# Performance work log

Measured on AMD Instinct MI355X. Metric: run time of the kernel, lower is better.

The kernel has to match this reference:

```python
import jax, jax.numpy as jnp
import numpy as np

N_NODES = 50000
N_FEAT = 256
N_HID = 256
N_CLASS = 40
N_EDGES = 800000


def setup_inputs() -> dict:
    key = jax.random.key(0)
    ks = jax.random.split(key, 12)
    x = jax.random.normal(ks[0], (N_NODES, N_FEAT), dtype=jnp.float32)
    edge_index = jax.random.randint(ks[1], (2, N_EDGES), 0, N_NODES, dtype=jnp.int64)
    def glorot(k, fan_in, fan_out):
        s = jnp.sqrt(6.0 / (fan_in + fan_out)).astype(jnp.float32)
        return jax.random.uniform(k, (fan_in, fan_out), jnp.float32, -s, s)
    return {
        "x": x,
        "edge_index": edge_index,
        "W1": glorot(ks[2], N_FEAT, N_HID), "b1": jnp.zeros((N_HID,), jnp.float32),
        "W2": glorot(ks[3], N_HID, N_HID), "b2": jnp.zeros((N_HID,), jnp.float32),
        "W3": glorot(ks[4], N_HID, N_HID), "b3": jnp.zeros((N_HID,), jnp.float32),
        "W4": glorot(ks[5], N_HID, N_CLASS), "b4": jnp.zeros((N_CLASS,), jnp.float32),
    }


def _gcn_norm(edge_index, num_nodes):
    # add self-loops, compute symmetric normalization (PyG gcn_norm)
    loop = jnp.arange(num_nodes, dtype=edge_index.dtype)
    src = jnp.concatenate([edge_index[0], loop])
    dst = jnp.concatenate([edge_index[1], loop])
    deg = jax.ops.segment_sum(jnp.ones_like(dst, dtype=jnp.float32), dst,
                              num_segments=num_nodes)
    dis = jnp.where(deg > 0, jax.lax.rsqrt(deg), 0.0)
    norm = dis[src] * dis[dst]  # [E + N]
    return src, dst, norm


def _gcn_conv(x, W, b, src, dst, norm, num_nodes):
    h = x @ W  # dense transform first (out_channels <= in_channels)
    msg = norm[:, None] * h[src]  # gather + scale
    out = jax.ops.segment_sum(msg, dst, num_segments=num_nodes)  # scatter-add
    return out + b


def reference(x, edge_index, W1, b1, W2, b2, W3, b3, W4, b4):
    n = x.shape[0]
    src, dst, norm = _gcn_norm(edge_index, n)
    h = jax.nn.relu(_gcn_conv(x, W1, b1, src, dst, norm, n))
    # dropout is identity in eval mode
    h = jax.nn.relu(_gcn_conv(h, W2, b2, src, dst, norm, n))
    h = jax.nn.relu(_gcn_conv(h, W3, b3, src, dst, norm, n))
    out = _gcn_conv(h, W4, b4, src, dst, norm, n)
    return out
```

## Files before the change

### kernel.cpp

```cpp
#include <hip/hip_runtime.h>

#define NN 50000
#define NF 256
#define NH 256
#define NC 40
#define NE 800000
#define CAP 64

typedef _Float16 f16x8 __attribute__((ext_vector_type(8)));
typedef float f32x4 __attribute__((ext_vector_type(4)));

__device__ __forceinline__ float f16f(unsigned short u) {
  union { unsigned short u; _Float16 h; } a; a.u = u;
  return (float)a.h;
}
__device__ __forceinline__ unsigned short f16u(float f) {
  union { unsigned short u; _Float16 h; } a; a.h = (_Float16)f;
  return a.u;
}

__device__ __forceinline__ void gl16(const void* g, void* l) {
  __builtin_amdgcn_global_load_lds(
      (const __attribute__((address_space(1))) unsigned int*)g,
      (__attribute__((address_space(3))) unsigned int*)l, 16, 0, 0);
}


__global__ void bucket_kernel(const int* __restrict__ src, const int* __restrict__ dst,
                              int* __restrict__ cnt, int* __restrict__ bucket) {
  int e = blockIdx.x * blockDim.x + threadIdx.x;
  if (e < NE) {
    int d = dst[e], s = src[e];
    int c = atomicAdd(&cnt[d], 1);
    if (c < CAP) bucket[(size_t)d * CAP + c] = s;
  }
}

__global__ void prep_kernel(const int* __restrict__ cnt, float* __restrict__ dis,
                            const float* __restrict__ W1, const float* __restrict__ W2,
                            const float* __restrict__ W3, const float* __restrict__ W4,
                            unsigned short* __restrict__ Wt1, unsigned short* __restrict__ Wt2,
                            unsigned short* __restrict__ Wt3, unsigned short* __restrict__ Wt4) {
  int idx = blockIdx.x * blockDim.x + threadIdx.x;
  if (idx < 262144) {
    const float* W; unsigned short* Wt; int N;
    if (idx < 65536)       { W = W1; Wt = Wt1; N = 256; }
    else if (idx < 131072) { W = W2; Wt = Wt2; N = 256; idx -= 65536; }
    else if (idx < 196608) { W = W3; Wt = Wt3; N = 256; idx -= 131072; }
    else                   { W = W4; Wt = Wt4; N = 40;  idx -= 196608; }
    int n = idx >> 8, k = idx & 255;
    float v = (n < N) ? W[k * N + n] : 0.0f;
    Wt[idx] = f16u(v);
  } else {
    int i = idx - 262144;
    if (i < NN) dis[i] = rsqrtf((float)(cnt[i] + 1));
  }
}


template <int NSTORE, bool AF32>
__global__ __launch_bounds__(256, 4) void gemm_f16(
    const void* __restrict__ Ain, const unsigned short* __restrict__ Bt,
    unsigned short* __restrict__ Cout, int M) {
  __shared__ unsigned short ldsA[64 * 64];
  __shared__ unsigned short ldsB[256 * 64];

  int tid = threadIdx.x;
  int rowBase = blockIdx.x * 64;
  int w = tid >> 6, lane = tid & 63;
  int l15 = lane & 15, l4 = lane >> 4;

  f32x4 acc[4][4] = {};

  for (int kt = 0; kt < 4; ++kt) {
#pragma unroll
    for (int c = 0; c < 2; ++c) {
      int gi = c * 256 + tid;
      int row = gi >> 3, gp = gi & 7;
      int gsrc = gp ^ (row & 7);
      int koff = kt * 64 + gsrc * 8;
      int ar = rowBase + row; ar = ar < M ? ar : M - 1;
      if (AF32) {
        const float* Af = (const float*)Ain + (size_t)ar * 256 + koff;
        float4 v0 = *(const float4*)Af;
        float4 v1 = *(const float4*)(Af + 4);
        f16x8 h = {(_Float16)v0.x, (_Float16)v0.y, (_Float16)v0.z, (_Float16)v0.w,
                   (_Float16)v1.x, (_Float16)v1.y, (_Float16)v1.z, (_Float16)v1.w};
        *(f16x8*)&ldsA[gi * 8] = h;
      } else {
        gl16((const unsigned short*)Ain + (size_t)ar * 256 + koff, &ldsA[gi * 8]);
      }
    }
#pragma unroll
    for (int c = 0; c < 8; ++c) {
      int gi = c * 256 + tid;
      int row = gi >> 3, gp = gi & 7;
      int gsrc = gp ^ (row & 7);
      int koff = kt * 64 + gsrc * 8;
      gl16(Bt + (size_t)row * 256 + koff, &ldsB[gi * 8]);
    }
    __syncthreads();

#pragma unroll
    for (int ks = 0; ks < 2; ++ks) {
      f16x8 a[4], b[4];
      int g = ks * 4 + l4;
#pragma unroll
      for (int mi = 0; mi < 4; ++mi) {
        int arow = mi * 16 + l15;
        int gp = g ^ (arow & 7);
        a[mi] = *(const f16x8*)&ldsA[arow * 64 + gp * 8];
      }
#pragma unroll
      for (int ni = 0; ni < 4; ++ni) {
        int brow = w * 64 + ni * 16 + l15;
        int gp = g ^ (brow & 7);
        b[ni] = *(const f16x8*)&ldsB[brow * 64 + gp * 8];
      }
#pragma unroll
      for (int mi = 0; mi < 4; ++mi)
#pragma unroll
        for (int ni = 0; ni < 4; ++ni)
          acc[mi][ni] = __builtin_amdgcn_mfma_f32_16x16x32_f16(a[mi], b[ni], acc[mi][ni], 0, 0, 0);
    }
    __syncthreads();
  }

#pragma unroll
  for (int ni = 0; ni < 4; ++ni) {
    int col = w * 64 + ni * 16 + l15;
    if (col < NSTORE) {
#pragma unroll
      for (int mi = 0; mi < 4; ++mi) {
        f32x4 v = acc[mi][ni];
#pragma unroll
        for (int i = 0; i < 4; ++i) {
          int r = rowBase + mi * 16 + l4 * 4 + i;
          if (r < M) Cout[(size_t)r * NSTORE + col] = f16u(v[i]);
        }
      }
    }
  }
}


__global__ __launch_bounds__(256) void agg256_kernel(
    const unsigned short* __restrict__ T, unsigned short* __restrict__ P,
    const int* __restrict__ cnt, const int* __restrict__ bucket,
    const float* __restrict__ dis, const float* __restrict__ b) {
  int node = (blockIdx.x * blockDim.x + threadIdx.x) >> 6;
  int lane = threadIdx.x & 63;
  if (node >= NN) return;
  const ushort4* Tv = (const ushort4*)T;
  float4 bv = ((const float4*)b)[lane];
  float d = dis[node];
  float w0 = d * d;
  ushort4 t = Tv[(size_t)node * 64 + lane];
  float ax = bv.x + w0 * f16f(t.x), ay = bv.y + w0 * f16f(t.y);
  float az = bv.z + w0 * f16f(t.z), aw = bv.w + w0 * f16f(t.w);
  int deg = cnt[node]; deg = deg < CAP ? deg : CAP;
  const int* bk = bucket + (size_t)node * CAP;
  int j = 0;
  for (; j + 4 <= deg; j += 4) {
    int s0 = bk[j], s1 = bk[j + 1], s2 = bk[j + 2], s3 = bk[j + 3];
    ushort4 t0 = Tv[(size_t)s0 * 64 + lane];
    ushort4 t1 = Tv[(size_t)s1 * 64 + lane];
    ushort4 t2 = Tv[(size_t)s2 * 64 + lane];
    ushort4 t3 = Tv[(size_t)s3 * 64 + lane];
    float f0 = d * dis[s0], f1 = d * dis[s1];
    float f2 = d * dis[s2], f3 = d * dis[s3];
    ax += f0 * f16f(t0.x) + f1 * f16f(t1.x) + f2 * f16f(t2.x) + f3 * f16f(t3.x);
    ay += f0 * f16f(t0.y) + f1 * f16f(t1.y) + f2 * f16f(t2.y) + f3 * f16f(t3.y);
    az += f0 * f16f(t0.z) + f1 * f16f(t1.z) + f2 * f16f(t2.z) + f3 * f16f(t3.z);
    aw += f0 * f16f(t0.w) + f1 * f16f(t1.w) + f2 * f16f(t2.w) + f3 * f16f(t3.w);
  }
  for (; j < deg; ++j) {
    int s = bk[j];
    float f = d * dis[s];
    ushort4 ts = Tv[(size_t)s * 64 + lane];
    ax += f * f16f(ts.x); ay += f * f16f(ts.y);
    az += f * f16f(ts.z); aw += f * f16f(ts.w);
  }
  ax = fmaxf(ax, 0.f); ay = fmaxf(ay, 0.f);
  az = fmaxf(az, 0.f); aw = fmaxf(aw, 0.f);
  ushort4 h;
  h.x = f16u(ax); h.y = f16u(ay); h.z = f16u(az); h.w = f16u(aw);
  ((ushort4*)P)[(size_t)node * 64 + lane] = h;
}

__global__ __launch_bounds__(256) void agg40_kernel(
    const unsigned short* __restrict__ T, float* __restrict__ O,
    const int* __restrict__ cnt, const int* __restrict__ bucket,
    const float* __restrict__ dis, const float* __restrict__ b) {
  int node = (blockIdx.x * blockDim.x + threadIdx.x) >> 6;
  int lane = threadIdx.x & 63;
  if (node >= NN) return;
  float d = dis[node];
  int deg = cnt[node]; deg = deg < CAP ? deg : CAP;
  const int* bk = bucket + (size_t)node * CAP;
  if (lane < NC) {
    float acc = b[lane] + d * d * f16f(T[(size_t)node * 64 + lane]);
    int j = 0;
    for (; j + 4 <= deg; j += 4) {
      int s0 = bk[j], s1 = bk[j + 1], s2 = bk[j + 2], s3 = bk[j + 3];
      float t0 = f16f(T[(size_t)s0 * 64 + lane]);
      float t1 = f16f(T[(size_t)s1 * 64 + lane]);
      float t2 = f16f(T[(size_t)s2 * 64 + lane]);
      float t3 = f16f(T[(size_t)s3 * 64 + lane]);
      acc += d * dis[s0] * t0 + d * dis[s1] * t1 + d * dis[s2] * t2 + d * dis[s3] * t3;
    }
    for (; j < deg; ++j) {
      int s = bk[j];
      acc += d * dis[s] * f16f(T[(size_t)s * 64 + lane]);
    }
    O[(size_t)node * NC + lane] = acc;
  }
}


extern "C" void kernel_launch(void* const* d_in, const int* in_sizes, int n_in,
                              void* d_out, int out_size, void* d_ws, size_t ws_size,
                              hipStream_t stream) {
  const float* x  = (const float*)d_in[0];
  const int* edge = (const int*)d_in[1];
  const float* W1 = (const float*)d_in[2];
  const float* b1 = (const float*)d_in[3];
  const float* W2 = (const float*)d_in[4];
  const float* b2 = (const float*)d_in[5];
  const float* W3 = (const float*)d_in[6];
  const float* b3 = (const float*)d_in[7];
  const float* W4 = (const float*)d_in[8];
  const float* b4 = (const float*)d_in[9];
  float* out = (float*)d_out;

  char* p = (char*)d_ws;
  unsigned short* T16 = (unsigned short*)p; p += (size_t)NN * NH * 2;
  unsigned short* P16 = (unsigned short*)p; p += (size_t)NN * NH * 2;
  int* cnt = (int*)p;                p += (size_t)NN * 4;
  float* dis = (float*)p;            p += (size_t)NN * 4;
  int* bucket = (int*)p;             p += (size_t)NN * CAP * 4;
  unsigned short* Wt1 = (unsigned short*)p; p += 256 * 256 * 2;
  unsigned short* Wt2 = (unsigned short*)p; p += 256 * 256 * 2;
  unsigned short* Wt3 = (unsigned short*)p; p += 256 * 256 * 2;
  unsigned short* Wt4 = (unsigned short*)p; p += 256 * 256 * 2;

  const int* e_src = edge;
  const int* e_dst = edge + NE;

  hipMemsetAsync(cnt, 0, (size_t)NN * 4, stream);

  bucket_kernel<<<(NE + 255) / 256, 256, 0, stream>>>(e_src, e_dst, cnt, bucket);
  prep_kernel<<<(262144 + NN + 255) / 256, 256, 0, stream>>>(cnt, dis, W1, W2, W3, W4,
                                                             Wt1, Wt2, Wt3, Wt4);

  int gemmBlocks = (NN + 63) / 64;
  int aggBlocks = (NN * 64 + 255) / 256;

  gemm_f16<256, true><<<gemmBlocks, 256, 0, stream>>>(x, Wt1, T16, NN);
  agg256_kernel<<<aggBlocks, 256, 0, stream>>>(T16, P16, cnt, bucket, dis, b1);
  gemm_f16<256, false><<<gemmBlocks, 256, 0, stream>>>(P16, Wt2, T16, NN);
  agg256_kernel<<<aggBlocks, 256, 0, stream>>>(T16, P16, cnt, bucket, dis, b2);
  gemm_f16<256, false><<<gemmBlocks, 256, 0, stream>>>(P16, Wt3, T16, NN);
  agg256_kernel<<<aggBlocks, 256, 0, stream>>>(T16, P16, cnt, bucket, dis, b3);
  gemm_f16<64, false><<<gemmBlocks, 256, 0, stream>>>(P16, Wt4, T16, NN);
  agg40_kernel<<<aggBlocks, 256, 0, stream>>>(T16, out, cnt, bucket, dis, b4);
}
```

Before: 336.0 us.

## Fuse edge bucketing into first GEMM launch and compute degree norms inline

Removes the memset, the standalone bucket kernel and the dis array. The prep kernel now zeroes cnt, and edge bucketing runs as extra blocks alongside the layer-1 GEMM in a single launch. The aggregation kernels recompute rsqrt(cnt+1) per neighbor instead of loading a precomputed dis array. This cuts launches and one pass, at the cost of extra rsqrt work per neighbor in every aggregation and heterogeneous blocks sharing one launch.

```diff
diff --git a/kernel.cpp b/kernel.cpp
--- a/kernel.cpp
+++ b/kernel.cpp
@@ -26,17 +26,7 @@
 }
 
 
-__global__ void bucket_kernel(const int* __restrict__ src, const int* __restrict__ dst,
-                              int* __restrict__ cnt, int* __restrict__ bucket) {
-  int e = blockIdx.x * blockDim.x + threadIdx.x;
-  if (e < NE) {
-    int d = dst[e], s = src[e];
-    int c = atomicAdd(&cnt[d], 1);
-    if (c < CAP) bucket[(size_t)d * CAP + c] = s;
-  }
-}
-
-__global__ void prep_kernel(const int* __restrict__ cnt, float* __restrict__ dis,
+__global__ void prep_kernel(int* __restrict__ cnt,
                             const float* __restrict__ W1, const float* __restrict__ W2,
                             const float* __restrict__ W3, const float* __restrict__ W4,
                             unsigned short* __restrict__ Wt1, unsigned short* __restrict__ Wt2,
@@ -53,20 +43,21 @@
     Wt[idx] = f16u(v);
   } else {
     int i = idx - 262144;
-    if (i < NN) dis[i] = rsqrtf((float)(cnt[i] + 1));
+    if (i < NN) cnt[i] = 0;
   }
 }
 
 
 template <int NSTORE, bool AF32>
-__global__ __launch_bounds__(256, 4) void gemm_f16(
-    const void* __restrict__ Ain, const unsigned short* __restrict__ Bt,
-    unsigned short* __restrict__ Cout, int M) {
+__device__ __forceinline__ void gemm_body(const void* __restrict__ Ain,
+                                          const unsigned short* __restrict__ Bt,
+                                          unsigned short* __restrict__ Cout,
+                                          int M, int blk) {
   __shared__ unsigned short ldsA[64 * 64];
   __shared__ unsigned short ldsB[256 * 64];
 
   int tid = threadIdx.x;
-  int rowBase = blockIdx.x * 64;
+  int rowBase = blk * 64;
   int w = tid >> 6, lane = tid & 63;
   int l15 = lane & 15, l4 = lane >> 4;
 
@@ -143,22 +134,51 @@
   }
 }
 
+#define GEMM_BLOCKS ((NN + 63) / 64)
+
+template <int NSTORE, bool AF32>
+__global__ __launch_bounds__(256, 4) void gemm_f16(
+    const void* __restrict__ Ain, const unsigned short* __restrict__ Bt,
+    unsigned short* __restrict__ Cout, int M) {
+  gemm_body<NSTORE, AF32>(Ain, Bt, Cout, M, blockIdx.x);
+}
+
+
+__global__ __launch_bounds__(256, 4) void fused1_kernel(
+    const float* __restrict__ x, const unsigned short* __restrict__ Wt1,
+    unsigned short* __restrict__ T16,
+    const int* __restrict__ src, const int* __restrict__ dst,
+    int* __restrict__ cnt, int* __restrict__ bucket) {
+  int bid = blockIdx.x;
+  if (bid < GEMM_BLOCKS) {
+    gemm_body<256, true>(x, Wt1, T16, NN, bid);
+  } else {
+    int e = (bid - GEMM_BLOCKS) * 256 + threadIdx.x;
+    if (e < NE) {
+      int d = dst[e], s = src[e];
+      int c = atomicAdd(&cnt[d], 1);
+      if (c < CAP) bucket[(size_t)d * CAP + c] = s;
+    }
+  }
+}
+
 
 __global__ __launch_bounds__(256) void agg256_kernel(
     const unsigned short* __restrict__ T, unsigned short* __restrict__ P,
     const int* __restrict__ cnt, const int* __restrict__ bucket,
-    const float* __restrict__ dis, const float* __restrict__ b) {
+    const float* __restrict__ b) {
   int node = (blockIdx.x * blockDim.x + threadIdx.x) >> 6;
   int lane = threadIdx.x & 63;
   if (node >= NN) return;
   const ushort4* Tv = (const ushort4*)T;
   float4 bv = ((const float4*)b)[lane];
-  float d = dis[node];
+  int cv = cnt[node];
+  float d = rsqrtf((float)(cv + 1));
+  int deg = cv < CAP ? cv : CAP;
   float w0 = d * d;
   ushort4 t = Tv[(size_t)node * 64 + lane];
   float ax = bv.x + w0 * f16f(t.x), ay = bv.y + w0 * f16f(t.y);
   float az = bv.z + w0 * f16f(t.z), aw = bv.w + w0 * f16f(t.w);
-  int deg = cnt[node]; deg = deg < CAP ? deg : CAP;
   const int* bk = bucket + (size_t)node * CAP;
   int j = 0;
   for (; j + 4 <= deg; j += 4) {
@@ -167,8 +187,10 @@
     ushort4 t1 = Tv[(size_t)s1 * 64 + lane];
     ushort4 t2 = Tv[(size_t)s2 * 64 + lane];
     ushort4 t3 = Tv[(size_t)s3 * 64 + lane];
-    float f0 = d * dis[s0], f1 = d * dis[s1];
-    float f2 = d * dis[s2], f3 = d * dis[s3];
+    float f0 = d * rsqrtf((float)(cnt[s0] + 1));
+    float f1 = d * rsqrtf((float)(cnt[s1] + 1));
+    float f2 = d * rsqrtf((float)(cnt[s2] + 1));
+    float f3 = d * rsqrtf((float)(cnt[s3] + 1));
     ax += f0 * f16f(t0.x) + f1 * f16f(t1.x) + f2 * f16f(t2.x) + f3 * f16f(t3.x);
     ay += f0 * f16f(t0.y) + f1 * f16f(t1.y) + f2 * f16f(t2.y) + f3 * f16f(t3.y);
     az += f0 * f16f(t0.z) + f1 * f16f(t1.z) + f2 * f16f(t2.z) + f3 * f16f(t3.z);
@@ -176,7 +198,7 @@
   }
   for (; j < deg; ++j) {
     int s = bk[j];
-    float f = d * dis[s];
+    float f = d * rsqrtf((float)(cnt[s] + 1));
     ushort4 ts = Tv[(size_t)s * 64 + lane];
     ax += f * f16f(ts.x); ay += f * f16f(ts.y);
     az += f * f16f(ts.z); aw += f * f16f(ts.w);
@@ -191,12 +213,13 @@
 __global__ __launch_bounds__(256) void agg40_kernel(
     const unsigned short* __restrict__ T, float* __restrict__ O,
     const int* __restrict__ cnt, const int* __restrict__ bucket,
-    const float* __restrict__ dis, const float* __restrict__ b) {
+    const float* __restrict__ b) {
   int node = (blockIdx.x * blockDim.x + threadIdx.x) >> 6;
   int lane = threadIdx.x & 63;
   if (node >= NN) return;
-  float d = dis[node];
-  int deg = cnt[node]; deg = deg < CAP ? deg : CAP;
+  int cv = cnt[node];
+  float d = rsqrtf((float)(cv + 1));
+  int deg = cv < CAP ? cv : CAP;
   const int* bk = bucket + (size_t)node * CAP;
   if (lane < NC) {
     float acc = b[lane] + d * d * f16f(T[(size_t)node * 64 + lane]);
@@ -207,11 +230,12 @@
       float t1 = f16f(T[(size_t)s1 * 64 + lane]);
       float t2 = f16f(T[(size_t)s2 * 64 + lane]);
       float t3 = f16f(T[(size_t)s3 * 64 + lane]);
-      acc += d * dis[s0] * t0 + d * dis[s1] * t1 + d * dis[s2] * t2 + d * dis[s3] * t3;
+      acc += d * rsqrtf((float)(cnt[s0] + 1)) * t0 + d * rsqrtf((float)(cnt[s1] + 1)) * t1 +
+             d * rsqrtf((float)(cnt[s2] + 1)) * t2 + d * rsqrtf((float)(cnt[s3] + 1)) * t3;
     }
     for (; j < deg; ++j) {
       int s = bk[j];
-      acc += d * dis[s] * f16f(T[(size_t)s * 64 + lane]);
+      acc += d * rsqrtf((float)(cnt[s] + 1)) * f16f(T[(size_t)s * 64 + lane]);
     }
     O[(size_t)node * NC + lane] = acc;
   }
@@ -237,7 +261,6 @@
   unsigned short* T16 = (unsigned short*)p; p += (size_t)NN * NH * 2;
   unsigned short* P16 = (unsigned short*)p; p += (size_t)NN * NH * 2;
   int* cnt = (int*)p;                p += (size_t)NN * 4;
-  float* dis = (float*)p;            p += (size_t)NN * 4;
   int* bucket = (int*)p;             p += (size_t)NN * CAP * 4;
   unsigned short* Wt1 = (unsigned short*)p; p += 256 * 256 * 2;
   unsigned short* Wt2 = (unsigned short*)p; p += 256 * 256 * 2;
@@ -247,21 +270,18 @@
   const int* e_src = edge;
   const int* e_dst = edge + NE;
 
-  hipMemsetAsync(cnt, 0, (size_t)NN * 4, stream);
-
-  bucket_kernel<<<(NE + 255) / 256, 256, 0, stream>>>(e_src, e_dst, cnt, bucket);
-  prep_kernel<<<(262144 + NN + 255) / 256, 256, 0, stream>>>(cnt, dis, W1, W2, W3, W4,
+  prep_kernel<<<(262144 + NN + 255) / 256, 256, 0, stream>>>(cnt, W1, W2, W3, W4,
                                                              Wt1, Wt2, Wt3, Wt4);
 
-  int gemmBlocks = (NN + 63) / 64;
+  int fusedBlocks = GEMM_BLOCKS + (NE + 255) / 256;
   int aggBlocks = (NN * 64 + 255) / 256;
 
-  gemm_f16<256, true><<<gemmBlocks, 256, 0, stream>>>(x, Wt1, T16, NN);
-  agg256_kernel<<<aggBlocks, 256, 0, stream>>>(T16, P16, cnt, bucket, dis, b1);
-  gemm_f16<256, false><<<gemmBlocks, 256, 0, stream>>>(P16, Wt2, T16, NN);
-  agg256_kernel<<<aggBlocks, 256, 0, stream>>>(T16, P16, cnt, bucket, dis, b2);
-  gemm_f16<256, false><<<gemmBlocks, 256, 0, stream>>>(P16, Wt3, T16, NN);
-  agg256_kernel<<<aggBlocks, 256, 0, stream>>>(T16, P16, cnt, bucket, dis, b3);
-  gemm_f16<64, false><<<gemmBlocks, 256, 0, stream>>>(P16, Wt4, T16, NN);
-  agg40_kernel<<<aggBlocks, 256, 0, stream>>>(T16, out, cnt, bucket, dis, b4);
-}
+  fused1_kernel<<<fusedBlocks, 256, 0, stream>>>(x, Wt1, T16, e_src, e_dst, cnt, bucket);
+  agg256_kernel<<<aggBlocks, 256, 0, stream>>>(T16, P16, cnt, bucket, b1);
+  gemm_f16<256, false><<<GEMM_BLOCKS, 256, 0, stream>>>(P16, Wt2, T16, NN);
+  agg256_kernel<<<aggBlocks, 256, 0, stream>>>(T16, P16, cnt, bucket, b2);
+  gemm_f16<256, false><<<GEMM_BLOCKS, 256, 0, stream>>>(P16, Wt3, T16, NN);
+  agg256_kernel<<<aggBlocks, 256, 0, stream>>>(T16, P16, cnt, bucket, b3);
+  gemm_f16<64, false><<<GEMM_BLOCKS, 256, 0, stream>>>(P16, Wt4, T16, NN);
+  agg40_kernel<<<aggBlocks, 256, 0, stream>>>(T16, out, cnt, bucket, b4);
+}
```

After: 341.9 us. About the same (+1.7%).
